# Kernel tuning notes

Measured on AMD Instinct MI355X. Metric: run time of the kernel, lower is better.

## Reference

```python
import jax, jax.numpy as jnp
import numpy as np

EPS = 1e-6

def setup_inputs() -> dict:
    key = jax.random.key(0)
    k1, k2 = jax.random.split(key)
    n, c, h, w = 16, 256, 64, 64
    n_F = w
    X = jax.random.normal(k1, (n, c, h, w), dtype=jnp.float32)
    # xavier_uniform for W [n_F, n_F]
    limit = float(np.sqrt(6.0 / (n_F + n_F)))
    W = jax.random.uniform(k2, (n_F, n_F), dtype=jnp.float32, minval=-limit, maxval=limit)
    a2 = jnp.ones((n_F,), dtype=jnp.float32)
    b2 = jnp.zeros((n_F,), dtype=jnp.float32)
    return {"X": X, "W": W, "a2": a2, "b2": b2}

def reference(X, W, a2, b2):
    n, c, h, w = X.shape
    Xf = X.reshape(n * c, h, w)                      # [nc, h, w]
    # attention-like matrix: transpose then softmax over last axis (length h)
    A = jax.nn.softmax(jnp.swapaxes(Xf, 1, 2), axis=2)  # [nc, w, h]
    # custom LayerNorm with unbiased std (torch x.std default, ddof=1)
    mean = jnp.mean(Xf, axis=-1, keepdims=True)
    std = jnp.std(Xf, axis=-1, ddof=1, keepdims=True)
    Xn = a2 * (Xf - mean) / (std + EPS) + b2          # [nc, h, w]
    node = jnp.matmul(A, Xn)                          # [nc, w, w]
    out = jax.nn.relu(jnp.matmul(node, W))            # [nc, w, w]
    return out.reshape(n, c, h, w)
```

## Files before the change

### kernel.cpp

```cpp
#include <hip/hip_runtime.h>

#define PAD 68

__global__ __launch_bounds__(256, 2)
void gnn_fused(const float* __restrict__ X, const float* __restrict__ W,
               const float* __restrict__ a2, const float* __restrict__ b2,
               float* __restrict__ out)
{
    __shared__ float Xs[64 * PAD];
    __shared__ float AT[64 * PAD];
    __shared__ float Ws[64 * PAD];
    __shared__ float a2s[64], b2s[64];

    const int tid = threadIdx.x;
    const int b   = blockIdx.x;
    const float* Xb = X + (size_t)b * 4096;

    #pragma unroll
    for (int i = 0; i < 4; ++i) {
        int f4  = tid + i * 256;
        int row = f4 >> 4;
        int col = (f4 & 15) << 2;
        float4 v  = ((const float4*)Xb)[f4];
        float4 wv = ((const float4*)W)[f4];
        *(float4*)&Xs[row * PAD + col] = v;
        *(float4*)&Ws[row * PAD + col] = wv;
    }
    if (tid < 64) { a2s[tid] = a2[tid]; b2s[tid] = b2[tid]; }
    __syncthreads();

    {
        const int col = tid >> 2;
        const int h0  = (tid & 3) << 4;
        float v[16];
        float m = -3.402823466e+38f;
        #pragma unroll
        for (int i = 0; i < 16; ++i) {
            v[i] = Xs[(h0 + i) * PAD + col];
            m = fmaxf(m, v[i]);
        }
        m = fmaxf(m, __shfl_xor(m, 1));
        m = fmaxf(m, __shfl_xor(m, 2));
        float s = 0.f;
        #pragma unroll
        for (int i = 0; i < 16; ++i) { v[i] = __expf(v[i] - m); s += v[i]; }
        s += __shfl_xor(s, 1);
        s += __shfl_xor(s, 2);
        const float inv = 1.0f / s;
        #pragma unroll
        for (int i = 0; i < 16; ++i) AT[(h0 + i) * PAD + col] = v[i] * inv;
    }
    __syncthreads();

    {
        const int row = tid >> 2;
        const int c0  = (tid & 3) << 4;
        float v[16];
        float s = 0.f, sq = 0.f;
        #pragma unroll
        for (int i = 0; i < 16; ++i) {
            v[i] = Xs[row * PAD + c0 + i];
            s  += v[i];
            sq += v[i] * v[i];
        }
        s  += __shfl_xor(s, 1);  s  += __shfl_xor(s, 2);
        sq += __shfl_xor(sq, 1); sq += __shfl_xor(sq, 2);
        const float mean = s * (1.0f / 64.0f);
        float var = (sq - 64.0f * mean * mean) * (1.0f / 63.0f);
        var = fmaxf(var, 0.0f);
        const float invstd = 1.0f / (sqrtf(var) + 1e-6f);
        #pragma unroll
        for (int i = 0; i < 16; ++i) {
            const int c = c0 + i;
            Xs[row * PAD + c] = a2s[c] * (v[i] - mean) * invstd + b2s[c];
        }
    }
    __syncthreads();

    const int ti = tid >> 4;
    const int tj = tid & 15;

    float acc[4][4];
    #pragma unroll
    for (int i = 0; i < 4; ++i)
        #pragma unroll
        for (int j = 0; j < 4; ++j) acc[i][j] = 0.f;

    #pragma unroll 8
    for (int k = 0; k < 64; ++k) {
        float4 xv = *(const float4*)&Xs[k * PAD + 4 * ti];
        float4 av = *(const float4*)&AT[k * PAD + 4 * tj];
        const float xr[4] = {xv.x, xv.y, xv.z, xv.w};
        const float ar[4] = {av.x, av.y, av.z, av.w};
        #pragma unroll
        for (int i = 0; i < 4; ++i)
            #pragma unroll
            for (int j = 0; j < 4; ++j) acc[i][j] += xr[i] * ar[j];
    }
    __syncthreads();
    #pragma unroll
    for (int i = 0; i < 4; ++i) {
        float4 v = make_float4(acc[i][0], acc[i][1], acc[i][2], acc[i][3]);
        *(float4*)&AT[(4 * ti + i) * PAD + 4 * tj] = v;
    }
    __syncthreads();

    float acc2[4][4];
    #pragma unroll
    for (int i = 0; i < 4; ++i)
        #pragma unroll
        for (int j = 0; j < 4; ++j) acc2[i][j] = 0.f;

    #pragma unroll 8
    for (int k = 0; k < 64; ++k) {
        float4 nv = *(const float4*)&AT[k * PAD + 4 * ti];
        float4 wv = *(const float4*)&Ws[k * PAD + 4 * tj];
        const float nr[4] = {nv.x, nv.y, nv.z, nv.w};
        const float wr[4] = {wv.x, wv.y, wv.z, wv.w};
        #pragma unroll
        for (int i = 0; i < 4; ++i)
            #pragma unroll
            for (int j = 0; j < 4; ++j) acc2[i][j] += nr[i] * wr[j];
    }

    float* outb = out + (size_t)b * 4096;
    #pragma unroll
    for (int i = 0; i < 4; ++i) {
        float4 v;
        v.x = fmaxf(acc2[i][0], 0.f);
        v.y = fmaxf(acc2[i][1], 0.f);
        v.z = fmaxf(acc2[i][2], 0.f);
        v.w = fmaxf(acc2[i][3], 0.f);
        *(float4*)&outb[(4 * ti + i) * 64 + 4 * tj] = v;
    }
}

extern "C" void kernel_launch(void* const* d_in, const int* in_sizes, int n_in,
                              void* d_out, int out_size, void* d_ws, size_t ws_size,
                              hipStream_t stream) {
    const float* X  = (const float*)d_in[0];
    const float* W  = (const float*)d_in[1];
    const float* a2 = (const float*)d_in[2];
    const float* b2 = (const float*)d_in[3];
    float* out = (float*)d_out;
    gnn_fused<<<4096, 256, 0, stream>>>(X, W, a2, b2, out);
}
```

Measured before the change: 157.3 us.

## Replace FP32 FMA matmuls with split-bf16 MFMA 32x32x16 and swizzled LDS

Both 64x64 matmuls per slice now run on MFMA bf16 instructions. Each fp32 operand is split into a high and a low bf16 part, and three MFMAs (hi*hi, hi*lo, lo*hi) recover near-fp32 accuracy. Operands are stored as bf16 in XOR-swizzled LDS, and X is read straight from global memory for the softmax and norm stages instead of being staged first. This cuts the scalar FMA work and LDS footprint so occupancy can rise to 3 blocks, at the cost of conversion overhead, uncoalesced scalar global reads and stores, and a small precision loss.

```diff
diff --git a/kernel.cpp b/kernel.cpp
--- a/kernel.cpp
+++ b/kernel.cpp
@@ -1,44 +1,45 @@
 #include <hip/hip_runtime.h>
 
-#define PAD 68
-
-__global__ __launch_bounds__(256, 2)
-void gnn_fused(const float* __restrict__ X, const float* __restrict__ W,
-               const float* __restrict__ a2, const float* __restrict__ b2,
-               float* __restrict__ out)
+
+typedef __attribute__((ext_vector_type(8)))  short  s16x8;
+typedef __attribute__((ext_vector_type(16))) float  f32x16;
+typedef __attribute__((ext_vector_type(8)))  unsigned short us8;
+
+__device__ __forceinline__ unsigned short f2bf(float x) {
+    unsigned u = __builtin_bit_cast(unsigned, x);
+    u += 0x7FFFu + ((u >> 16) & 1u);
+    return (unsigned short)(u >> 16);
+}
+__device__ __forceinline__ float bf2f(unsigned short h) {
+    unsigned u = ((unsigned)h) << 16;
+    return __builtin_bit_cast(float, u);
+}
+__device__ __forceinline__ int swidx(int row, int k) {
+    return row * 64 + (k ^ ((row & 7) << 3));
+}
+
+__global__ __launch_bounds__(256, 3)
+void gnn_mfma(const float* __restrict__ X, const float* __restrict__ Wg,
+              const float* __restrict__ a2, const float* __restrict__ b2,
+              float* __restrict__ out)
 {
-    __shared__ float Xs[64 * PAD];
-    __shared__ float AT[64 * PAD];
-    __shared__ float Ws[64 * PAD];
-    __shared__ float a2s[64], b2s[64];
+    __shared__ __align__(16) unsigned short bufA[2][64 * 64];
+    __shared__ __align__(16) unsigned short bufX[2][64 * 64];
+    __shared__ __align__(16) unsigned short bufW[2][64 * 64];
 
     const int tid = threadIdx.x;
     const int b   = blockIdx.x;
-    const float* Xb = X + (size_t)b * 4096;
-
-    #pragma unroll
-    for (int i = 0; i < 4; ++i) {
-        int f4  = tid + i * 256;
-        int row = f4 >> 4;
-        int col = (f4 & 15) << 2;
-        float4 v  = ((const float4*)Xb)[f4];
-        float4 wv = ((const float4*)W)[f4];
-        *(float4*)&Xs[row * PAD + col] = v;
-        *(float4*)&Ws[row * PAD + col] = wv;
-    }
-    if (tid < 64) { a2s[tid] = a2[tid]; b2s[tid] = b2[tid]; }
-    __syncthreads();
+    const float* xb = X + (size_t)b * 4096;
 
     {
-        const int col = tid >> 2;
-        const int h0  = (tid & 3) << 4;
+        const int wi = tid >> 2;
+        const int h0 = (tid & 3) << 4;
         float v[16];
-        float m = -3.402823466e+38f;
-        #pragma unroll
-        for (int i = 0; i < 16; ++i) {
-            v[i] = Xs[(h0 + i) * PAD + col];
-            m = fmaxf(m, v[i]);
-        }
+        #pragma unroll
+        for (int i = 0; i < 16; ++i) v[i] = xb[(h0 + i) * 64 + wi];
+        float m = v[0];
+        #pragma unroll
+        for (int i = 1; i < 16; ++i) m = fmaxf(m, v[i]);
         m = fmaxf(m, __shfl_xor(m, 1));
         m = fmaxf(m, __shfl_xor(m, 2));
         float s = 0.f;
@@ -47,91 +48,147 @@
         s += __shfl_xor(s, 1);
         s += __shfl_xor(s, 2);
         const float inv = 1.0f / s;
-        #pragma unroll
-        for (int i = 0; i < 16; ++i) AT[(h0 + i) * PAD + col] = v[i] * inv;
-    }
-    __syncthreads();
+        us8 hv0, lv0, hv1, lv1;
+        #pragma unroll
+        for (int i = 0; i < 8; ++i) {
+            float p = v[i] * inv;
+            unsigned short hh = f2bf(p);
+            hv0[i] = hh; lv0[i] = f2bf(p - bf2f(hh));
+        }
+        #pragma unroll
+        for (int i = 0; i < 8; ++i) {
+            float p = v[8 + i] * inv;
+            unsigned short hh = f2bf(p);
+            hv1[i] = hh; lv1[i] = f2bf(p - bf2f(hh));
+        }
+        const int sw = (wi & 7) << 3;
+        const int i0 = wi * 64 + (h0 ^ sw);
+        const int i1 = wi * 64 + ((h0 + 8) ^ sw);
+        *(us8*)&bufA[0][i0] = hv0; *(us8*)&bufA[0][i1] = hv1;
+        *(us8*)&bufA[1][i0] = lv0; *(us8*)&bufA[1][i1] = lv1;
+    }
 
     {
-        const int row = tid >> 2;
-        const int c0  = (tid & 3) << 4;
-        float v[16];
+        const int h  = tid >> 2;
+        const int c0 = (tid & 3) << 4;
+        float x[16];
+        #pragma unroll
+        for (int i = 0; i < 4; ++i) {
+            float4 t = *(const float4*)&xb[h * 64 + c0 + 4 * i];
+            x[4 * i] = t.x; x[4 * i + 1] = t.y; x[4 * i + 2] = t.z; x[4 * i + 3] = t.w;
+        }
         float s = 0.f, sq = 0.f;
         #pragma unroll
-        for (int i = 0; i < 16; ++i) {
-            v[i] = Xs[row * PAD + c0 + i];
-            s  += v[i];
-            sq += v[i] * v[i];
-        }
+        for (int i = 0; i < 16; ++i) { s += x[i]; sq += x[i] * x[i]; }
         s  += __shfl_xor(s, 1);  s  += __shfl_xor(s, 2);
         sq += __shfl_xor(sq, 1); sq += __shfl_xor(sq, 2);
         const float mean = s * (1.0f / 64.0f);
         float var = (sq - 64.0f * mean * mean) * (1.0f / 63.0f);
         var = fmaxf(var, 0.0f);
         const float invstd = 1.0f / (sqrtf(var) + 1e-6f);
+        float av[16], bv[16];
+        #pragma unroll
+        for (int i = 0; i < 4; ++i) {
+            float4 ta = *(const float4*)&a2[c0 + 4 * i];
+            float4 tb = *(const float4*)&b2[c0 + 4 * i];
+            av[4*i] = ta.x; av[4*i+1] = ta.y; av[4*i+2] = ta.z; av[4*i+3] = ta.w;
+            bv[4*i] = tb.x; bv[4*i+1] = tb.y; bv[4*i+2] = tb.z; bv[4*i+3] = tb.w;
+        }
         #pragma unroll
         for (int i = 0; i < 16; ++i) {
-            const int c = c0 + i;
-            Xs[row * PAD + c] = a2s[c] * (v[i] - mean) * invstd + b2s[c];
-        }
+            float xn = av[i] * (x[i] - mean) * invstd + bv[i];
+            unsigned short hh = f2bf(xn);
+            const int idx = swidx(c0 + i, h);
+            bufX[0][idx] = hh;
+            bufX[1][idx] = f2bf(xn - bf2f(hh));
+        }
+    }
+
+    {
+        const int j = tid & 63;
+        const int q = tid >> 6;
+        float wv[16];
+        #pragma unroll
+        for (int i = 0; i < 16; ++i) wv[i] = Wg[(16 * q + i) * 64 + j];
+        us8 hv0, lv0, hv1, lv1;
+        #pragma unroll
+        for (int i = 0; i < 8; ++i) {
+            unsigned short hh = f2bf(wv[i]);
+            hv0[i] = hh; lv0[i] = f2bf(wv[i] - bf2f(hh));
+        }
+        #pragma unroll
+        for (int i = 0; i < 8; ++i) {
+            unsigned short hh = f2bf(wv[8 + i]);
+            hv1[i] = hh; lv1[i] = f2bf(wv[8 + i] - bf2f(hh));
+        }
+        const int sw = (j & 7) << 3;
+        const int i0 = j * 64 + ((16 * q) ^ sw);
+        const int i1 = j * 64 + ((16 * q + 8) ^ sw);
+        *(us8*)&bufW[0][i0] = hv0; *(us8*)&bufW[0][i1] = hv1;
+        *(us8*)&bufW[1][i0] = lv0; *(us8*)&bufW[1][i1] = lv1;
     }
     __syncthreads();
 
-    const int ti = tid >> 4;
-    const int tj = tid & 15;
-
-    float acc[4][4];
-    #pragma unroll
-    for (int i = 0; i < 4; ++i)
-        #pragma unroll
-        for (int j = 0; j < 4; ++j) acc[i][j] = 0.f;
-
-    #pragma unroll 8
-    for (int k = 0; k < 64; ++k) {
-        float4 xv = *(const float4*)&Xs[k * PAD + 4 * ti];
-        float4 av = *(const float4*)&AT[k * PAD + 4 * tj];
-        const float xr[4] = {xv.x, xv.y, xv.z, xv.w};
-        const float ar[4] = {av.x, av.y, av.z, av.w};
-        #pragma unroll
-        for (int i = 0; i < 4; ++i)
-            #pragma unroll
-            for (int j = 0; j < 4; ++j) acc[i][j] += xr[i] * ar[j];
+    const int wid  = tid >> 6;
+    const int lane = tid & 63;
+    const int r    = lane & 31;
+    const int hl   = lane >> 5;
+    const int R = (wid & 1) * 32;
+    const int C = (wid >> 1) * 32;
+
+    f32x16 acc;
+    #pragma unroll
+    for (int i = 0; i < 16; ++i) acc[i] = 0.f;
+
+    const int rowA = R + r;
+    const int rowB = C + r;
+    #pragma unroll
+    for (int t = 0; t < 4; ++t) {
+        const int k0 = 16 * t + 8 * hl;
+        s16x8 aH = *(const s16x8*)&bufA[0][rowA * 64 + (k0 ^ ((rowA & 7) << 3))];
+        s16x8 aL = *(const s16x8*)&bufA[1][rowA * 64 + (k0 ^ ((rowA & 7) << 3))];
+        s16x8 bH = *(const s16x8*)&bufX[0][rowB * 64 + (k0 ^ ((rowB & 7) << 3))];
+        s16x8 bL = *(const s16x8*)&bufX[1][rowB * 64 + (k0 ^ ((rowB & 7) << 3))];
+        acc = __builtin_amdgcn_mfma_f32_32x32x16_bf16(aH, bH, acc, 0, 0, 0);
+        acc = __builtin_amdgcn_mfma_f32_32x32x16_bf16(aH, bL, acc, 0, 0, 0);
+        acc = __builtin_amdgcn_mfma_f32_32x32x16_bf16(aL, bH, acc, 0, 0, 0);
     }
     __syncthreads();
-    #pragma unroll
-    for (int i = 0; i < 4; ++i) {
-        float4 v = make_float4(acc[i][0], acc[i][1], acc[i][2], acc[i][3]);
-        *(float4*)&AT[(4 * ti + i) * PAD + 4 * tj] = v;
+
+    #pragma unroll
+    for (int g = 0; g < 16; ++g) {
+        const int w1 = R + (g & 3) + 8 * (g >> 2) + 4 * hl;
+        const float xv = acc[g];
+        const unsigned short hh = f2bf(xv);
+        const int idx = swidx(w1, C + r);
+        bufA[0][idx] = hh;
+        bufA[1][idx] = f2bf(xv - bf2f(hh));
     }
     __syncthreads();
 
-    float acc2[4][4];
-    #pragma unroll
-    for (int i = 0; i < 4; ++i)
-        #pragma unroll
-        for (int j = 0; j < 4; ++j) acc2[i][j] = 0.f;
-
-    #pragma unroll 8
-    for (int k = 0; k < 64; ++k) {
-        float4 nv = *(const float4*)&AT[k * PAD + 4 * ti];
-        float4 wv = *(const float4*)&Ws[k * PAD + 4 * tj];
-        const float nr[4] = {nv.x, nv.y, nv.z, nv.w};
-        const float wr[4] = {wv.x, wv.y, wv.z, wv.w};
-        #pragma unroll
-        for (int i = 0; i < 4; ++i)
-            #pragma unroll
-            for (int j = 0; j < 4; ++j) acc2[i][j] += nr[i] * wr[j];
-    }
-
-    float* outb = out + (size_t)b * 4096;
-    #pragma unroll
-    for (int i = 0; i < 4; ++i) {
-        float4 v;
-        v.x = fmaxf(acc2[i][0], 0.f);
-        v.y = fmaxf(acc2[i][1], 0.f);
-        v.z = fmaxf(acc2[i][2], 0.f);
-        v.w = fmaxf(acc2[i][3], 0.f);
-        *(float4*)&outb[(4 * ti + i) * 64 + 4 * tj] = v;
+    f32x16 acc2;
+    #pragma unroll
+    for (int i = 0; i < 16; ++i) acc2[i] = 0.f;
+
+    const int rowN = R + r;
+    const int rowW = C + r;
+    #pragma unroll
+    for (int t = 0; t < 4; ++t) {
+        const int k0 = 16 * t + 8 * hl;
+        s16x8 nH = *(const s16x8*)&bufA[0][rowN * 64 + (k0 ^ ((rowN & 7) << 3))];
+        s16x8 nL = *(const s16x8*)&bufA[1][rowN * 64 + (k0 ^ ((rowN & 7) << 3))];
+        s16x8 wH = *(const s16x8*)&bufW[0][rowW * 64 + (k0 ^ ((rowW & 7) << 3))];
+        s16x8 wL = *(const s16x8*)&bufW[1][rowW * 64 + (k0 ^ ((rowW & 7) << 3))];
+        acc2 = __builtin_amdgcn_mfma_f32_32x32x16_bf16(nH, wH, acc2, 0, 0, 0);
+        acc2 = __builtin_amdgcn_mfma_f32_32x32x16_bf16(nH, wL, acc2, 0, 0, 0);
+        acc2 = __builtin_amdgcn_mfma_f32_32x32x16_bf16(nL, wH, acc2, 0, 0, 0);
+    }
+
+    float* ob = out + (size_t)b * 4096;
+    #pragma unroll
+    for (int g = 0; g < 16; ++g) {
+        const int w1 = R + (g & 3) + 8 * (g >> 2) + 4 * hl;
+        ob[w1 * 64 + C + r] = fmaxf(acc2[g], 0.f);
     }
 }
 
@@ -143,5 +200,5 @@
     const float* a2 = (const float*)d_in[2];
     const float* b2 = (const float*)d_in[3];
     float* out = (float*)d_out;
-    gnn_fused<<<4096, 256, 0, stream>>>(X, W, a2, b2, out);
-}
+    gnn_mfma<<<4096, 256, 0, stream>>>(X, W, a2, b2, out);
+}
```

Measured after the change: 136.6 us. 1.15x faster.
